# Optimization experiments

Measured on AMD Instinct MI355X. Metric: run time of the kernel, lower is better.

Reference implementation:

```python
import jax, jax.numpy as jnp
import numpy as np

N, E, C_IN, C_OUT, G = 100000, 1250000, 64, 64, 64
H = 2 * C_OUT  # hidden width of conv1 output


def _lin(k, out_d, in_d, scale=0.05):
    kw, kb = jax.random.split(k)
    return (jax.random.normal(kw, (out_d, in_d), jnp.float32) * scale,
            jax.random.normal(kb, (out_d,), jnp.float32) * scale)


def setup_inputs() -> dict:
    key = jax.random.key(0)
    ks = jax.random.split(key, 12)
    x = jax.random.normal(ks[0], (N, C_IN), jnp.float32)
    edge_index = jax.random.randint(ks[1], (2, E), 0, N, jnp.int64)
    batch = jnp.sort(jax.random.randint(ks[2], (N,), 0, G, jnp.int64))
    # GraphConv layer 1: lin_rel (with bias) on aggregated msgs, lin_root (no bias) on x
    w1_rel, b1_rel = _lin(ks[3], H, C_IN)
    w1_root = jax.random.normal(ks[4], (H, C_IN), jnp.float32) * 0.05
    # GraphConv layer 2
    w2_rel, b2_rel = _lin(ks[5], C_OUT, H)
    w2_root = jax.random.normal(ks[6], (C_OUT, H), jnp.float32) * 0.05
    # encoder_S: out_channels -> 8 -> 4 -> 1
    es_w1, es_b1 = _lin(ks[7], 8, C_OUT)
    es_w2, es_b2 = _lin(ks[8], 4, 8)
    es_w3, es_b3 = _lin(ks[9], 1, 4)
    # decoder: 1 -> 4 -> 8 -> out_channels (input dim fixed from buggy 2 to 1)
    d_w1, d_b1 = _lin(ks[10], 4, 1)
    d_w2, d_b2 = _lin(ks[11], 8, 4)
    d_w3, d_b3 = _lin(jax.random.fold_in(key, 99), C_OUT, 8)
    return dict(x=x, edge_index=edge_index, batch=batch,
                w1_rel=w1_rel, b1_rel=b1_rel, w1_root=w1_root,
                w2_rel=w2_rel, b2_rel=b2_rel, w2_root=w2_root,
                es_w1=es_w1, es_b1=es_b1, es_w2=es_w2, es_b2=es_b2,
                es_w3=es_w3, es_b3=es_b3,
                d_w1=d_w1, d_b1=d_b1, d_w2=d_w2, d_b2=d_b2,
                d_w3=d_w3, d_b3=d_b3)


def reference(x, edge_index, batch,
              w1_rel, b1_rel, w1_root,
              w2_rel, b2_rel, w2_root,
              es_w1, es_b1, es_w2, es_b2, es_w3, es_b3,
              d_w1, d_b1, d_w2, d_b2, d_w3, d_b3):
    src, dst = edge_index[0], edge_index[1]
    # GraphConv 1: sum-aggregate source feats into targets, then rel+root linears
    agg1 = jax.ops.segment_sum(x[src], dst, num_segments=N)  # [N, C_IN]
    h1 = jax.nn.relu(agg1 @ w1_rel.T + b1_rel + x @ w1_root.T)  # [N, H]
    # GraphConv 2
    agg2 = jax.ops.segment_sum(h1[src], dst, num_segments=N)
    h2 = jax.nn.relu(agg2 @ w2_rel.T + b2_rel + h1 @ w2_root.T)  # [N, C_OUT]
    # global mean pool over graphs
    counts = jax.ops.segment_sum(jnp.ones((N,), h2.dtype), batch, num_segments=G)
    h3 = jax.ops.segment_sum(h2, batch, num_segments=G) / jnp.maximum(counts, 1.0)[:, None]  # [G, C_OUT]
    # encoder_S MLP -> z
    z = jax.nn.relu(h3 @ es_w1.T + es_b1)
    z = jax.nn.relu(z @ es_w2.T + es_b2)
    z = z @ es_w3.T + es_b3  # [G, 1]
    # decoder MLP -> x_
    x_ = jax.nn.relu(z @ d_w1.T + d_b1)
    x_ = jax.nn.relu(x_ @ d_w2.T + d_b2)
    x_ = x_ @ d_w3.T + d_b3  # [G, C_OUT]
    return h3, x_
```

## Files before the change

kernel.cpp:

```cpp
#include <hip/hip_runtime.h>
#include <stdint.h>

#define NN 100000
#define EE 1250000
#define NBUCK 196
#define CHUNK 4096
#define NCHUNK ((EE + CHUNK - 1) / CHUNK)
#define PSLICE 24

typedef __attribute__((ext_vector_type(8))) short short8;
typedef __attribute__((ext_vector_type(4))) float f32x4;

__device__ inline ushort f2bf(float f) {
  union { float f; uint32_t u; } v; v.f = f;
  uint32_t r = v.u + 0x7FFF + ((v.u >> 16) & 1);
  return (ushort)(r >> 16);
}
__device__ inline float bf2f(ushort h) {
  union { uint32_t u; float f; } v; v.u = ((uint32_t)h) << 16;
  return v.f;
}

__global__ __launch_bounds__(256) void kprepfrag(const float* __restrict__ w1_rel,
                                                 const float* __restrict__ w1_root,
                                                 const float* __restrict__ w2_rel,
                                                 const float* __restrict__ w2_root,
                                                 ushort* __restrict__ WF) {
  int idx = blockIdx.x * 256 + threadIdx.x;
  if (idx >= 8192) return;
  int j = idx & 7, l = (idx >> 3) & 63, ts = idx >> 9;
  {
    int s = ts & 1, t = ts >> 1;
    int o = t * 16 + (l & 15), k = s * 32 + (l >> 4) * 8 + j;
    WF[idx] = f2bf(w1_rel[o * 64 + k]);
    WF[8192 + idx] = f2bf(w1_root[o * 64 + k]);
  }
  {
    int s = ts & 3, t = ts >> 2;
    int o = t * 16 + (l & 15), k = s * 32 + (l >> 4) * 8 + j;
    WF[16384 + idx] = f2bf(w2_rel[o * 128 + k]);
    WF[24576 + idx] = f2bf(w2_root[o * 128 + k]);
  }
}

__global__ __launch_bounds__(256) void kxcvt(const float* __restrict__ x,
                                             ushort* __restrict__ xb) {
  int i = (blockIdx.x * 256 + threadIdx.x) * 4;
  if (i >= NN * 64) return;
  float4 v = *reinterpret_cast<const float4*>(x + i);
  ushort o[4] = {f2bf(v.x), f2bf(v.y), f2bf(v.z), f2bf(v.w)};
  *reinterpret_cast<uint2*>(xb + i) = *reinterpret_cast<uint2*>(o);
}

__global__ __launch_bounds__(256) void kbinA1(const int* __restrict__ dstI,
                                              int* __restrict__ histG) {
  __shared__ int h[NBUCK];
  int t = threadIdx.x;
  if (t < NBUCK) h[t] = 0;
  __syncthreads();
  int cb = blockIdx.x * CHUNK;
  int cc = EE - cb; if (cc > CHUNK) cc = CHUNK;
  for (int i = t; i < cc; i += 256) atomicAdd(&h[dstI[cb + i] >> 9], 1);
  __syncthreads();
  if (t < NBUCK) histG[blockIdx.x * NBUCK + t] = h[t];
}

__global__ __launch_bounds__(512) void kscan2d(const int* __restrict__ histG,
                                               int* __restrict__ relG,
                                               int* __restrict__ bucketTotal) {
  __shared__ int sm[512];
  int b = blockIdx.x;
  int t = threadIdx.x;
  int v = (t < NCHUNK) ? histG[t * NBUCK + b] : 0;
  sm[t] = v;
  __syncthreads();
  for (int d = 1; d < 512; d <<= 1) {
    int u = (t >= d) ? sm[t - d] : 0;
    __syncthreads();
    sm[t] += u;
    __syncthreads();
  }
  if (t < NCHUNK) relG[t * NBUCK + b] = sm[t] - v;
  if (t == 511) bucketTotal[b] = sm[511];
}

__global__ __launch_bounds__(256) void kscan196(const int* __restrict__ bucketTotal,
                                                int* __restrict__ bucketStart) {
  __shared__ int ss[256];
  int t = threadIdx.x;
  int v = (t < NBUCK) ? bucketTotal[t] : 0;
  ss[t] = v;
  __syncthreads();
  for (int d = 1; d < 256; d <<= 1) {
    int u = (t >= d) ? ss[t - d] : 0;
    __syncthreads();
    ss[t] += u;
    __syncthreads();
  }
  if (t < NBUCK) bucketStart[t] = ss[t] - v;
  if (t == NBUCK - 1) bucketStart[NBUCK] = ss[t];
}

__global__ __launch_bounds__(256) void kbinA2(const int* __restrict__ srcI,
                                              const int* __restrict__ dstI,
                                              const int* __restrict__ histG,
                                              const int* __restrict__ relG,
                                              const int* __restrict__ bucketStart,
                                              uint32_t* __restrict__ pairsG) {
  __shared__ uint32_t pko[CHUNK];
  __shared__ int ss[256];
  __shared__ int ex[NBUCK + 1];
  __shared__ int cur[NBUCK];
  __shared__ int gb[NBUCK];
  int t = threadIdx.x;
  int cb = blockIdx.x * CHUNK;
  int cc = EE - cb; if (cc > CHUNK) cc = CHUNK;

  int v = (t < NBUCK) ? histG[blockIdx.x * NBUCK + t] : 0;
  ss[t] = v;
  __syncthreads();
  for (int d = 1; d < 256; d <<= 1) {
    int u = (t >= d) ? ss[t - d] : 0;
    __syncthreads();
    ss[t] += u;
    __syncthreads();
  }
  if (t < NBUCK) {
    ex[t] = ss[t] - v;
    cur[t] = ss[t] - v;
    gb[t] = bucketStart[t] + relG[blockIdx.x * NBUCK + t];
  }
  if (t == NBUCK - 1) ex[NBUCK] = ss[t];
  __syncthreads();
  for (int i = t; i < cc; i += 256) {
    int d = dstI[cb + i];
    int s = srcI[cb + i];
    int b = d >> 9;
    int p = atomicAdd(&cur[b], 1);
    pko[p] = (uint32_t)s | ((uint32_t)(d & 511) << 17);
  }
  __syncthreads();
  if (t < NBUCK) {
    int base = ex[t], cnt = ex[t + 1] - base, g0 = gb[t];
    for (int j = 0; j < cnt; ++j) pairsG[g0 + j] = pko[base + j];
  }
}

__global__ __launch_bounds__(256) void kbinB(const uint32_t* __restrict__ pairsG,
                                             const int* __restrict__ bucketStart,
                                             int* __restrict__ starts,
                                             int* __restrict__ esrc) {
  __shared__ int hist[512];
  __shared__ int ex2[512];
  __shared__ int part[256];
  int t = threadIdx.x;
  int b = blockIdx.x;
  int nbase = b << 9;
  int base = bucketStart[b];
  int ecnt = bucketStart[b + 1] - base;

  hist[t] = 0; hist[t + 256] = 0;
  __syncthreads();
  for (int i = t; i < ecnt; i += 256) atomicAdd(&hist[pairsG[base + i] >> 17], 1);
  __syncthreads();
  int a = hist[2 * t], c = hist[2 * t + 1];
  part[t] = a + c;
  __syncthreads();
  for (int d = 1; d < 256; d <<= 1) {
    int u = (t >= d) ? part[t - d] : 0;
    __syncthreads();
    part[t] += u;
    __syncthreads();
  }
  int pex = part[t] - (a + c);
  ex2[2 * t] = pex;
  ex2[2 * t + 1] = pex + a;
  __syncthreads();
  for (int n = t; n < 512; n += 256) {
    int node = nbase + n;
    if (node < NN) starts[node] = base + ex2[n];
  }
  if (b == NBUCK - 1 && t == 0) starts[NN] = EE;
  for (int n = t; n < 512; n += 256) hist[n] = ex2[n];
  __syncthreads();
  for (int i = t; i < ecnt; i += 256) {
    uint32_t p = pairsG[base + i];
    int dl = p >> 17;
    int s = p & 0x1FFFF;
    int lp = atomicAdd(&hist[dl], 1);
    esrc[base + lp] = s;
  }
}

__global__ __launch_bounds__(256) void kgatherQ(const ushort* __restrict__ featb,
                                                const int* __restrict__ starts,
                                                const int* __restrict__ esrc,
                                                ushort* __restrict__ outb) {
  int w = (blockIdx.x * 256 + threadIdx.x) >> 4;
  if (w >= NN) return;
  int lq = threadIdx.x & 15;
  int b = starts[w], e = starts[w + 1];
  float a0 = 0.f, a1 = 0.f, a2 = 0.f, a3 = 0.f;
  int i = b;
  int s0 = 0, s1 = 0, s2 = 0, s3 = 0;
  bool have = (i + 4 <= e);
  if (have) { s0 = esrc[i]; s1 = esrc[i + 1]; s2 = esrc[i + 2]; s3 = esrc[i + 3]; }
  while (have) {
    uint2 u0 = *(const uint2*)(featb + (size_t)s0 * 64 + 4 * lq);
    uint2 u1 = *(const uint2*)(featb + (size_t)s1 * 64 + 4 * lq);
    uint2 u2 = *(const uint2*)(featb + (size_t)s2 * 64 + 4 * lq);
    uint2 u3 = *(const uint2*)(featb + (size_t)s3 * 64 + 4 * lq);
    i += 4;
    have = (i + 4 <= e);
    if (have) { s0 = esrc[i]; s1 = esrc[i + 1]; s2 = esrc[i + 2]; s3 = esrc[i + 3]; }
    a0 += bf2f((ushort)u0.x) + bf2f((ushort)u1.x) + bf2f((ushort)u2.x) + bf2f((ushort)u3.x);
    a1 += bf2f((ushort)(u0.x >> 16)) + bf2f((ushort)(u1.x >> 16)) +
          bf2f((ushort)(u2.x >> 16)) + bf2f((ushort)(u3.x >> 16));
    a2 += bf2f((ushort)u0.y) + bf2f((ushort)u1.y) + bf2f((ushort)u2.y) + bf2f((ushort)u3.y);
    a3 += bf2f((ushort)(u0.y >> 16)) + bf2f((ushort)(u1.y >> 16)) +
          bf2f((ushort)(u2.y >> 16)) + bf2f((ushort)(u3.y >> 16));
  }
  for (; i < e; ++i) {
    int s = esrc[i];
    uint2 u = *(const uint2*)(featb + (size_t)s * 64 + 4 * lq);
    a0 += bf2f((ushort)u.x); a1 += bf2f((ushort)(u.x >> 16));
    a2 += bf2f((ushort)u.y); a3 += bf2f((ushort)(u.y >> 16));
  }
  uint2 o;
  o.x = (uint32_t)f2bf(a0) | ((uint32_t)f2bf(a1) << 16);
  o.y = (uint32_t)f2bf(a2) | ((uint32_t)f2bf(a3) << 16);
  *(uint2*)(outb + (size_t)w * 64 + 4 * lq) = o;
}

__global__ __launch_bounds__(256) void kgh2Q(const ushort* __restrict__ featb,
                                             const int* __restrict__ starts,
                                             const int* __restrict__ esrc,
                                             const ushort* __restrict__ r2b,
                                             const float* __restrict__ b2v,
                                             ushort* __restrict__ h2b) {
  int w = (blockIdx.x * 256 + threadIdx.x) >> 4;
  if (w >= NN) return;
  int lq = threadIdx.x & 15;
  int b = starts[w], e = starts[w + 1];
  float a0 = 0.f, a1 = 0.f, a2 = 0.f, a3 = 0.f;
  int i = b;
  int s0 = 0, s1 = 0, s2 = 0, s3 = 0;
  bool have = (i + 4 <= e);
  if (have) { s0 = esrc[i]; s1 = esrc[i + 1]; s2 = esrc[i + 2]; s3 = esrc[i + 3]; }
  while (have) {
    uint2 u0 = *(const uint2*)(featb + (size_t)s0 * 64 + 4 * lq);
    uint2 u1 = *(const uint2*)(featb + (size_t)s1 * 64 + 4 * lq);
    uint2 u2 = *(const uint2*)(featb + (size_t)s2 * 64 + 4 * lq);
    uint2 u3 = *(const uint2*)(featb + (size_t)s3 * 64 + 4 * lq);
    i += 4;
    have = (i + 4 <= e);
    if (have) { s0 = esrc[i]; s1 = esrc[i + 1]; s2 = esrc[i + 2]; s3 = esrc[i + 3]; }
    a0 += bf2f((ushort)u0.x) + bf2f((ushort)u1.x) + bf2f((ushort)u2.x) + bf2f((ushort)u3.x);
    a1 += bf2f((ushort)(u0.x >> 16)) + bf2f((ushort)(u1.x >> 16)) +
          bf2f((ushort)(u2.x >> 16)) + bf2f((ushort)(u3.x >> 16));
    a2 += bf2f((ushort)u0.y) + bf2f((ushort)u1.y) + bf2f((ushort)u2.y) + bf2f((ushort)u3.y);
    a3 += bf2f((ushort)(u0.y >> 16)) + bf2f((ushort)(u1.y >> 16)) +
          bf2f((ushort)(u2.y >> 16)) + bf2f((ushort)(u3.y >> 16));
  }
  for (; i < e; ++i) {
    int s = esrc[i];
    uint2 u = *(const uint2*)(featb + (size_t)s * 64 + 4 * lq);
    a0 += bf2f((ushort)u.x); a1 += bf2f((ushort)(u.x >> 16));
    a2 += bf2f((ushort)u.y); a3 += bf2f((ushort)(u.y >> 16));
  }
  uint2 ru = *(const uint2*)(r2b + (size_t)w * 64 + 4 * lq);
  float4 bias = *(const float4*)(b2v + 4 * lq);
  float v0 = fmaxf(a0 + bf2f((ushort)ru.x) + bias.x, 0.f);
  float v1 = fmaxf(a1 + bf2f((ushort)(ru.x >> 16)) + bias.y, 0.f);
  float v2 = fmaxf(a2 + bf2f((ushort)ru.y) + bias.z, 0.f);
  float v3 = fmaxf(a3 + bf2f((ushort)(ru.y >> 16)) + bias.w, 0.f);
  uint2 o;
  o.x = (uint32_t)f2bf(v0) | ((uint32_t)f2bf(v1) << 16);
  o.y = (uint32_t)f2bf(v2) | ((uint32_t)f2bf(v3) << 16);
  *(uint2*)(h2b + (size_t)w * 64 + 4 * lq) = o;
}

__global__ __launch_bounds__(256) void kfused(const ushort* __restrict__ xb,
                                              const ushort* __restrict__ aggb,
                                              const ushort* __restrict__ WF,
                                              const float* __restrict__ b1,
                                              ushort* __restrict__ y,
                                              ushort* __restrict__ r2b) {
  __shared__ __align__(16) char hT[16384];
  int t = threadIdx.x, l = t & 63, wv = t >> 6;
  int n0 = blockIdx.x * 64 + wv * 16;
  int row = l & 15;
  int kg = l >> 4;
  int nr = n0 + row; if (nr > NN - 1) nr = NN - 1;

  short8 aA[2], aX[2];
  {
    const ushort* ap = aggb + (size_t)nr * 64 + kg * 8;
    aA[0] = *(const short8*)(ap);
    aA[1] = *(const short8*)(ap + 32);
    const ushort* xp = xb + (size_t)nr * 64 + kg * 8;
    aX[0] = *(const short8*)(xp);
    aX[1] = *(const short8*)(xp + 32);
  }

  const ushort* wf1rel = WF;
  const ushort* wf1root = WF + 8192;
  char* basep = hT + wv * 4096;

#pragma unroll
  for (int tt = 0; tt < 8; ++tt) {
    f32x4 acc = {0.f, 0.f, 0.f, 0.f};
#pragma unroll
    for (int s = 0; s < 2; ++s) {
      short8 br = *(const short8*)(wf1rel + ((size_t)(tt * 2 + s) * 64 + l) * 8);
      acc = __builtin_amdgcn_mfma_f32_16x16x32_bf16(aA[s], br, acc, 0, 0, 0);
      short8 bo = *(const short8*)(wf1root + ((size_t)(tt * 2 + s) * 64 + l) * 8);
      acc = __builtin_amdgcn_mfma_f32_16x16x32_bf16(aX[s], bo, acc, 0, 0, 0);
    }
    float bias = b1[tt * 16 + row];
#pragma unroll
    for (int r = 0; r < 4; ++r) {
      float hv = fmaxf(acc[r] + bias, 0.f);
      int nl = kg * 4 + r;
      int off = nl * 256 + (tt * 16 + row) * 2;
      off ^= (nl & 7) << 4;
      *(ushort*)(basep + off) = f2bf(hv);
    }
  }
  __syncthreads();

  short8 aH[4];
#pragma unroll
  for (int s = 0; s < 4; ++s) {
    int off = row * 256 + s * 64 + kg * 16;
    off ^= (row & 7) << 4;
    aH[s] = *(const short8*)(basep + off);
  }

  const ushort* wf2rel = WF + 16384;
  const ushort* wf2root = WF + 24576;
#pragma unroll
  for (int tt = 0; tt < 4; ++tt) {
    f32x4 accY = {0.f, 0.f, 0.f, 0.f};
    f32x4 accR = {0.f, 0.f, 0.f, 0.f};
#pragma unroll
    for (int s = 0; s < 4; ++s) {
      short8 br = *(const short8*)(wf2rel + ((size_t)(tt * 4 + s) * 64 + l) * 8);
      accY = __builtin_amdgcn_mfma_f32_16x16x32_bf16(aH[s], br, accY, 0, 0, 0);
      short8 bo = *(const short8*)(wf2root + ((size_t)(tt * 4 + s) * 64 + l) * 8);
      accR = __builtin_amdgcn_mfma_f32_16x16x32_bf16(aH[s], bo, accR, 0, 0, 0);
    }
#pragma unroll
    for (int r = 0; r < 4; ++r) {
      int nd = n0 + kg * 4 + r;
      if (nd < NN) {
        y[(size_t)nd * 64 + tt * 16 + row] = f2bf(accY[r]);
        r2b[(size_t)nd * 64 + tt * 16 + row] = f2bf(accR[r]);
      }
    }
  }
}

__global__ __launch_bounds__(256) void kpoolpart(const ushort* __restrict__ h2b,
                                                 const int* __restrict__ batch,
                                                 float* __restrict__ poolP) {
  __shared__ int gbs[2];
  __shared__ float part[4][64];
  int g = blockIdx.x / PSLICE, sl = blockIdx.x % PSLICE;
  int t = threadIdx.x;
  if (t < 2) {
    int target = g + t;
    int lo = 0, hi = NN;
    while (lo < hi) { int m = (lo + hi) >> 1; if (batch[m] < target) lo = m + 1; else hi = m; }
    gbs[t] = lo;
  }
  __syncthreads();
  int n0 = gbs[0], len = gbs[1] - n0;
  int lo = n0 + (int)((long)len * sl / PSLICE);
  int hi = n0 + (int)((long)len * (sl + 1) / PSLICE);
  int ch = t & 63, sub = t >> 6;
  float acc = 0.f;
  int n = lo + sub;
  for (; n + 12 < hi; n += 16) {
    float v0 = bf2f(h2b[(size_t)n * 64 + ch]);
    float v1 = bf2f(h2b[(size_t)(n + 4) * 64 + ch]);
    float v2 = bf2f(h2b[(size_t)(n + 8) * 64 + ch]);
    float v3 = bf2f(h2b[(size_t)(n + 12) * 64 + ch]);
    acc += (v0 + v1) + (v2 + v3);
  }
  for (; n < hi; n += 4) acc += bf2f(h2b[(size_t)n * 64 + ch]);
  part[sub][ch] = acc;
  __syncthreads();
  if (t < 64)
    poolP[(size_t)blockIdx.x * 64 + t] = part[0][t] + part[1][t] + part[2][t] + part[3][t];
}

__global__ __launch_bounds__(64) void kfinal3(
    const float* __restrict__ poolP, const int* __restrict__ batch,
    const float* __restrict__ es_w1, const float* __restrict__ es_b1,
    const float* __restrict__ es_w2, const float* __restrict__ es_b2,
    const float* __restrict__ es_w3, const float* __restrict__ es_b3,
    const float* __restrict__ d_w1, const float* __restrict__ d_b1,
    const float* __restrict__ d_w2, const float* __restrict__ d_b2,
    const float* __restrict__ d_w3, const float* __restrict__ d_b3,
    float* __restrict__ out) {
  __shared__ float h3[64];
  __shared__ float z1s[8];
  __shared__ float t2s[8];
  __shared__ int gbs[2];
  int g = blockIdx.x;
  int l = threadIdx.x;
  if (l < 2) {
    int target = g + l;
    int lo = 0, hi = NN;
    while (lo < hi) { int m = (lo + hi) >> 1; if (batch[m] < target) lo = m + 1; else hi = m; }
    gbs[l] = lo;
  }
  float s = 0.f;
#pragma unroll
  for (int k = 0; k < PSLICE; ++k) s += poolP[(size_t)(g * PSLICE + k) * 64 + l];
  __syncthreads();
  float c = fmaxf((float)(gbs[1] - gbs[0]), 1.f);
  float h = s / c;
  h3[l] = h;
  out[g * 64 + l] = h;
  __syncthreads();
  if (l < 8) {
    float a = es_b1[l];
#pragma unroll
    for (int k = 0; k < 64; ++k) a += es_w1[l * 64 + k] * h3[k];
    z1s[l] = fmaxf(a, 0.f);
  }
  __syncthreads();
  if (l == 0) {
    float z2[4];
#pragma unroll
    for (int j = 0; j < 4; ++j) {
      float a = es_b2[j];
#pragma unroll
      for (int k = 0; k < 8; ++k) a += es_w2[j * 8 + k] * z1s[k];
      z2[j] = fmaxf(a, 0.f);
    }
    float z = es_b3[0];
#pragma unroll
    for (int k = 0; k < 4; ++k) z += es_w3[k] * z2[k];
    float t1[4];
#pragma unroll
    for (int j = 0; j < 4; ++j) t1[j] = fmaxf(d_w1[j] * z + d_b1[j], 0.f);
#pragma unroll
    for (int j = 0; j < 8; ++j) {
      float a = d_b2[j];
#pragma unroll
      for (int k = 0; k < 4; ++k) a += d_w2[j * 4 + k] * t1[k];
      t2s[j] = fmaxf(a, 0.f);
    }
  }
  __syncthreads();
  float a = d_b3[l];
#pragma unroll
  for (int k = 0; k < 8; ++k) a += d_w3[l * 8 + k] * t2s[k];
  out[4096 + g * 64 + l] = a;
}

extern "C" void kernel_launch(void* const* d_in, const int* in_sizes, int n_in,
                              void* d_out, int out_size, void* d_ws, size_t ws_size,
                              hipStream_t stream) {
  const float* x = (const float*)d_in[0];
  const int* ei = (const int*)d_in[1];
  const int* srcI = ei;
  const int* dstI = ei + EE;
  const int* batch = (const int*)d_in[2];
  const float* w1_rel = (const float*)d_in[3];
  const float* b1_rel = (const float*)d_in[4];
  const float* w1_root = (const float*)d_in[5];
  const float* w2_rel = (const float*)d_in[6];
  const float* b2_rel = (const float*)d_in[7];
  const float* w2_root = (const float*)d_in[8];
  const float* es_w1 = (const float*)d_in[9];
  const float* es_b1 = (const float*)d_in[10];
  const float* es_w2 = (const float*)d_in[11];
  const float* es_b2 = (const float*)d_in[12];
  const float* es_w3 = (const float*)d_in[13];
  const float* es_b3 = (const float*)d_in[14];
  const float* d_w1 = (const float*)d_in[15];
  const float* d_b1 = (const float*)d_in[16];
  const float* d_w2 = (const float*)d_in[17];
  const float* d_b2 = (const float*)d_in[18];
  const float* d_w3 = (const float*)d_in[19];
  const float* d_b3 = (const float*)d_in[20];

  ushort* xb = (ushort*)d_ws;
  ushort* aggb = xb + (size_t)NN * 64;
  ushort* yb = aggb + (size_t)NN * 64;
  ushort* r2b = yb + (size_t)NN * 64;
  ushort* h2b = r2b + (size_t)NN * 64;
  ushort* WF = h2b + (size_t)NN * 64;
  float* poolP = (float*)(WF + 32768);
  int* starts = (int*)(poolP + 64 * PSLICE * 64);
  int* histG = starts + NN + 1;
  int* relG = histG + NCHUNK * NBUCK;
  int* bucketTotal = relG + NCHUNK * NBUCK;
  int* bucketStart = bucketTotal + NBUCK;
  uint32_t* pairsG = (uint32_t*)(bucketStart + NBUCK + 1);
  int* esrc = (int*)(pairsG + EE);
  float* out = (float*)d_out;

  kprepfrag<<<32, 256, 0, stream>>>(w1_rel, w1_root, w2_rel, w2_root, WF);
  kxcvt<<<(NN * 64 / 4 + 255) / 256, 256, 0, stream>>>(x, xb);
  kbinA1<<<NCHUNK, 256, 0, stream>>>(dstI, histG);
  kscan2d<<<NBUCK, 512, 0, stream>>>(histG, relG, bucketTotal);
  kscan196<<<1, 256, 0, stream>>>(bucketTotal, bucketStart);
  kbinA2<<<NCHUNK, 256, 0, stream>>>(srcI, dstI, histG, relG, bucketStart, pairsG);
  kbinB<<<NBUCK, 256, 0, stream>>>(pairsG, bucketStart, starts, esrc);
  kgatherQ<<<(NN * 16 + 255) / 256, 256, 0, stream>>>(xb, starts, esrc, aggb);
  kfused<<<(NN + 63) / 64, 256, 0, stream>>>(xb, aggb, WF, b1_rel, yb, r2b);
  kgh2Q<<<(NN * 16 + 255) / 256, 256, 0, stream>>>(yb, starts, esrc, r2b, b2_rel, h2b);
  kpoolpart<<<64 * PSLICE, 256, 0, stream>>>(h2b, batch, poolP);
  kfinal3<<<64, 64, 0, stream>>>(poolP, batch, es_w1, es_b1, es_w2, es_b2, es_w3, es_b3,
                                 d_w1, d_b1, d_w2, d_b2, d_w3, d_b3, out);
}
```

Baseline: 148.9 us.

## Merge front-end prep kernels, deepen gather unroll, double rows per wave in kfused

Folds the weight-fragment prep, x-to-bf16 conversion and destination histogram kernels into one launch that dispatches on block index, removing two kernel launches and their gaps. The two gather kernels share a macro that prefetches eight edge indices per iteration and handles the tail in 4/2/1 steps, raising memory-level parallelism per lane. The fused MLP kernel now processes 32 rows per wave with a 32KB LDS buffer, reusing each loaded weight fragment twice at the cost of more registers and LDS, which may reduce occupancy.

```diff
diff --git a/kernel.cpp b/kernel.cpp
--- a/kernel.cpp
+++ b/kernel.cpp
@@ -7,6 +7,7 @@
 #define CHUNK 4096
 #define NCHUNK ((EE + CHUNK - 1) / CHUNK)
 #define PSLICE 24
+#define XB_NB ((NN * 64 / 4 + 255) / 256)
 
 typedef __attribute__((ext_vector_type(8))) short short8;
 typedef __attribute__((ext_vector_type(4))) float f32x4;
@@ -21,48 +22,52 @@
   return v.f;
 }
 
-__global__ __launch_bounds__(256) void kprepfrag(const float* __restrict__ w1_rel,
-                                                 const float* __restrict__ w1_root,
-                                                 const float* __restrict__ w2_rel,
-                                                 const float* __restrict__ w2_root,
-                                                 ushort* __restrict__ WF) {
-  int idx = blockIdx.x * 256 + threadIdx.x;
-  if (idx >= 8192) return;
-  int j = idx & 7, l = (idx >> 3) & 63, ts = idx >> 9;
-  {
-    int s = ts & 1, t = ts >> 1;
-    int o = t * 16 + (l & 15), k = s * 32 + (l >> 4) * 8 + j;
-    WF[idx] = f2bf(w1_rel[o * 64 + k]);
-    WF[8192 + idx] = f2bf(w1_root[o * 64 + k]);
-  }
-  {
-    int s = ts & 3, t = ts >> 2;
-    int o = t * 16 + (l & 15), k = s * 32 + (l >> 4) * 8 + j;
-    WF[16384 + idx] = f2bf(w2_rel[o * 128 + k]);
-    WF[24576 + idx] = f2bf(w2_root[o * 128 + k]);
-  }
-}
-
-__global__ __launch_bounds__(256) void kxcvt(const float* __restrict__ x,
-                                             ushort* __restrict__ xb) {
-  int i = (blockIdx.x * 256 + threadIdx.x) * 4;
-  if (i >= NN * 64) return;
-  float4 v = *reinterpret_cast<const float4*>(x + i);
-  ushort o[4] = {f2bf(v.x), f2bf(v.y), f2bf(v.z), f2bf(v.w)};
-  *reinterpret_cast<uint2*>(xb + i) = *reinterpret_cast<uint2*>(o);
-}
-
-__global__ __launch_bounds__(256) void kbinA1(const int* __restrict__ dstI,
+__global__ __launch_bounds__(256) void kfront(const float* __restrict__ w1_rel,
+                                              const float* __restrict__ w1_root,
+                                              const float* __restrict__ w2_rel,
+                                              const float* __restrict__ w2_root,
+                                              const float* __restrict__ x,
+                                              const int* __restrict__ dstI,
+                                              ushort* __restrict__ WF,
+                                              ushort* __restrict__ xb,
                                               int* __restrict__ histG) {
   __shared__ int h[NBUCK];
   int t = threadIdx.x;
-  if (t < NBUCK) h[t] = 0;
-  __syncthreads();
-  int cb = blockIdx.x * CHUNK;
-  int cc = EE - cb; if (cc > CHUNK) cc = CHUNK;
-  for (int i = t; i < cc; i += 256) atomicAdd(&h[dstI[cb + i] >> 9], 1);
-  __syncthreads();
-  if (t < NBUCK) histG[blockIdx.x * NBUCK + t] = h[t];
+  int blk = blockIdx.x;
+  if (blk < 32) {
+    int idx = blk * 256 + t;
+    if (idx < 8192) {
+      int j = idx & 7, l = (idx >> 3) & 63, ts = idx >> 9;
+      {
+        int s = ts & 1, tt = ts >> 1;
+        int o = tt * 16 + (l & 15), k = s * 32 + (l >> 4) * 8 + j;
+        WF[idx] = f2bf(w1_rel[o * 64 + k]);
+        WF[8192 + idx] = f2bf(w1_root[o * 64 + k]);
+      }
+      {
+        int s = ts & 3, tt = ts >> 2;
+        int o = tt * 16 + (l & 15), k = s * 32 + (l >> 4) * 8 + j;
+        WF[16384 + idx] = f2bf(w2_rel[o * 128 + k]);
+        WF[24576 + idx] = f2bf(w2_root[o * 128 + k]);
+      }
+    }
+  } else if (blk < 32 + XB_NB) {
+    int i = ((blk - 32) * 256 + t) * 4;
+    if (i < NN * 64) {
+      float4 v = *reinterpret_cast<const float4*>(x + i);
+      ushort o[4] = {f2bf(v.x), f2bf(v.y), f2bf(v.z), f2bf(v.w)};
+      *reinterpret_cast<uint2*>(xb + i) = *reinterpret_cast<uint2*>(o);
+    }
+  } else {
+    int c = blk - 32 - XB_NB;
+    if (t < NBUCK) h[t] = 0;
+    __syncthreads();
+    int cb = c * CHUNK;
+    int cc = EE - cb; if (cc > CHUNK) cc = CHUNK;
+    for (int i = t; i < cc; i += 256) atomicAdd(&h[dstI[cb + i] >> 9], 1);
+    __syncthreads();
+    if (t < NBUCK) histG[c * NBUCK + t] = h[t];
+  }
 }
 
 __global__ __launch_bounds__(512) void kscan2d(const int* __restrict__ histG,
@@ -192,6 +197,79 @@
   }
 }
 
+#define GATHER_CORE(featb)                                                         \
+  float a0 = 0.f, a1 = 0.f, a2 = 0.f, a3 = 0.f;                                    \
+  const ushort* fb = (featb) + 4 * lq;                                             \
+  int i = b;                                                                       \
+  {                                                                                \
+    int s0 = 0, s1 = 0, s2 = 0, s3 = 0, s4 = 0, s5 = 0, s6 = 0, s7 = 0;            \
+    bool have = (i + 8 <= e);                                                      \
+    if (have) {                                                                    \
+      s0 = esrc[i];     s1 = esrc[i + 1]; s2 = esrc[i + 2]; s3 = esrc[i + 3];      \
+      s4 = esrc[i + 4]; s5 = esrc[i + 5]; s6 = esrc[i + 6]; s7 = esrc[i + 7];      \
+    }                                                                              \
+    while (have) {                                                                 \
+      uint2 u0 = *(const uint2*)(fb + (size_t)s0 * 64);                            \
+      uint2 u1 = *(const uint2*)(fb + (size_t)s1 * 64);                            \
+      uint2 u2 = *(const uint2*)(fb + (size_t)s2 * 64);                            \
+      uint2 u3 = *(const uint2*)(fb + (size_t)s3 * 64);                            \
+      uint2 u4 = *(const uint2*)(fb + (size_t)s4 * 64);                            \
+      uint2 u5 = *(const uint2*)(fb + (size_t)s5 * 64);                            \
+      uint2 u6 = *(const uint2*)(fb + (size_t)s6 * 64);                            \
+      uint2 u7 = *(const uint2*)(fb + (size_t)s7 * 64);                            \
+      i += 8;                                                                      \
+      have = (i + 8 <= e);                                                         \
+      if (have) {                                                                  \
+        s0 = esrc[i];     s1 = esrc[i + 1]; s2 = esrc[i + 2]; s3 = esrc[i + 3];    \
+        s4 = esrc[i + 4]; s5 = esrc[i + 5]; s6 = esrc[i + 6]; s7 = esrc[i + 7];    \
+      }                                                                            \
+      a0 += bf2f((ushort)u0.x) + bf2f((ushort)u1.x) + bf2f((ushort)u2.x) +         \
+            bf2f((ushort)u3.x) + bf2f((ushort)u4.x) + bf2f((ushort)u5.x) +         \
+            bf2f((ushort)u6.x) + bf2f((ushort)u7.x);                               \
+      a1 += bf2f((ushort)(u0.x >> 16)) + bf2f((ushort)(u1.x >> 16)) +              \
+            bf2f((ushort)(u2.x >> 16)) + bf2f((ushort)(u3.x >> 16)) +              \
+            bf2f((ushort)(u4.x >> 16)) + bf2f((ushort)(u5.x >> 16)) +              \
+            bf2f((ushort)(u6.x >> 16)) + bf2f((ushort)(u7.x >> 16));               \
+      a2 += bf2f((ushort)u0.y) + bf2f((ushort)u1.y) + bf2f((ushort)u2.y) +         \
+            bf2f((ushort)u3.y) + bf2f((ushort)u4.y) + bf2f((ushort)u5.y) +         \
+            bf2f((ushort)u6.y) + bf2f((ushort)u7.y);                               \
+      a3 += bf2f((ushort)(u0.y >> 16)) + bf2f((ushort)(u1.y >> 16)) +              \
+            bf2f((ushort)(u2.y >> 16)) + bf2f((ushort)(u3.y >> 16)) +              \
+            bf2f((ushort)(u4.y >> 16)) + bf2f((ushort)(u5.y >> 16)) +              \
+            bf2f((ushort)(u6.y >> 16)) + bf2f((ushort)(u7.y >> 16));               \
+    }                                                                              \
+  }                                                                                \
+  if (i + 4 <= e) {                                                                \
+    int s0 = esrc[i], s1 = esrc[i + 1], s2 = esrc[i + 2], s3 = esrc[i + 3];        \
+    uint2 u0 = *(const uint2*)(fb + (size_t)s0 * 64);                              \
+    uint2 u1 = *(const uint2*)(fb + (size_t)s1 * 64);                              \
+    uint2 u2 = *(const uint2*)(fb + (size_t)s2 * 64);                              \
+    uint2 u3 = *(const uint2*)(fb + (size_t)s3 * 64);                              \
+    a0 += bf2f((ushort)u0.x) + bf2f((ushort)u1.x) + bf2f((ushort)u2.x) + bf2f((ushort)u3.x); \
+    a1 += bf2f((ushort)(u0.x >> 16)) + bf2f((ushort)(u1.x >> 16)) +                \
+          bf2f((ushort)(u2.x >> 16)) + bf2f((ushort)(u3.x >> 16));                 \
+    a2 += bf2f((ushort)u0.y) + bf2f((ushort)u1.y) + bf2f((ushort)u2.y) + bf2f((ushort)u3.y); \
+    a3 += bf2f((ushort)(u0.y >> 16)) + bf2f((ushort)(u1.y >> 16)) +                \
+          bf2f((ushort)(u2.y >> 16)) + bf2f((ushort)(u3.y >> 16));                 \
+    i += 4;                                                                        \
+  }                                                                                \
+  if (i + 2 <= e) {                                                                \
+    int s0 = esrc[i], s1 = esrc[i + 1];                                            \
+    uint2 u0 = *(const uint2*)(fb + (size_t)s0 * 64);                              \
+    uint2 u1 = *(const uint2*)(fb + (size_t)s1 * 64);                              \
+    a0 += bf2f((ushort)u0.x) + bf2f((ushort)u1.x);                                 \
+    a1 += bf2f((ushort)(u0.x >> 16)) + bf2f((ushort)(u1.x >> 16));                 \
+    a2 += bf2f((ushort)u0.y) + bf2f((ushort)u1.y);                                 \
+    a3 += bf2f((ushort)(u0.y >> 16)) + bf2f((ushort)(u1.y >> 16));                 \
+    i += 2;                                                                        \
+  }                                                                                \
+  if (i < e) {                                                                     \
+    int s0 = esrc[i];                                                              \
+    uint2 u0 = *(const uint2*)(fb + (size_t)s0 * 64);                              \
+    a0 += bf2f((ushort)u0.x); a1 += bf2f((ushort)(u0.x >> 16));                    \
+    a2 += bf2f((ushort)u0.y); a3 += bf2f((ushort)(u0.y >> 16));                    \
+  }
+
 __global__ __launch_bounds__(256) void kgatherQ(const ushort* __restrict__ featb,
                                                 const int* __restrict__ starts,
                                                 const int* __restrict__ esrc,
@@ -200,32 +278,7 @@
   if (w >= NN) return;
   int lq = threadIdx.x & 15;
   int b = starts[w], e = starts[w + 1];
-  float a0 = 0.f, a1 = 0.f, a2 = 0.f, a3 = 0.f;
-  int i = b;
-  int s0 = 0, s1 = 0, s2 = 0, s3 = 0;
-  bool have = (i + 4 <= e);
-  if (have) { s0 = esrc[i]; s1 = esrc[i + 1]; s2 = esrc[i + 2]; s3 = esrc[i + 3]; }
-  while (have) {
-    uint2 u0 = *(const uint2*)(featb + (size_t)s0 * 64 + 4 * lq);
-    uint2 u1 = *(const uint2*)(featb + (size_t)s1 * 64 + 4 * lq);
-    uint2 u2 = *(const uint2*)(featb + (size_t)s2 * 64 + 4 * lq);
-    uint2 u3 = *(const uint2*)(featb + (size_t)s3 * 64 + 4 * lq);
-    i += 4;
-    have = (i + 4 <= e);
-    if (have) { s0 = esrc[i]; s1 = esrc[i + 1]; s2 = esrc[i + 2]; s3 = esrc[i + 3]; }
-    a0 += bf2f((ushort)u0.x) + bf2f((ushort)u1.x) + bf2f((ushort)u2.x) + bf2f((ushort)u3.x);
-    a1 += bf2f((ushort)(u0.x >> 16)) + bf2f((ushort)(u1.x >> 16)) +
-          bf2f((ushort)(u2.x >> 16)) + bf2f((ushort)(u3.x >> 16));
-    a2 += bf2f((ushort)u0.y) + bf2f((ushort)u1.y) + bf2f((ushort)u2.y) + bf2f((ushort)u3.y);
-    a3 += bf2f((ushort)(u0.y >> 16)) + bf2f((ushort)(u1.y >> 16)) +
-          bf2f((ushort)(u2.y >> 16)) + bf2f((ushort)(u3.y >> 16));
-  }
-  for (; i < e; ++i) {
-    int s = esrc[i];
-    uint2 u = *(const uint2*)(featb + (size_t)s * 64 + 4 * lq);
-    a0 += bf2f((ushort)u.x); a1 += bf2f((ushort)(u.x >> 16));
-    a2 += bf2f((ushort)u.y); a3 += bf2f((ushort)(u.y >> 16));
-  }
+  GATHER_CORE(featb)
   uint2 o;
   o.x = (uint32_t)f2bf(a0) | ((uint32_t)f2bf(a1) << 16);
   o.y = (uint32_t)f2bf(a2) | ((uint32_t)f2bf(a3) << 16);
@@ -242,32 +295,7 @@
   if (w >= NN) return;
   int lq = threadIdx.x & 15;
   int b = starts[w], e = starts[w + 1];
-  float a0 = 0.f, a1 = 0.f, a2 = 0.f, a3 = 0.f;
-  int i = b;
-  int s0 = 0, s1 = 0, s2 = 0, s3 = 0;
-  bool have = (i + 4 <= e);
-  if (have) { s0 = esrc[i]; s1 = esrc[i + 1]; s2 = esrc[i + 2]; s3 = esrc[i + 3]; }
-  while (have) {
-    uint2 u0 = *(const uint2*)(featb + (size_t)s0 * 64 + 4 * lq);
-    uint2 u1 = *(const uint2*)(featb + (size_t)s1 * 64 + 4 * lq);
-    uint2 u2 = *(const uint2*)(featb + (size_t)s2 * 64 + 4 * lq);
-    uint2 u3 = *(const uint2*)(featb + (size_t)s3 * 64 + 4 * lq);
-    i += 4;
-    have = (i + 4 <= e);
-    if (have) { s0 = esrc[i]; s1 = esrc[i + 1]; s2 = esrc[i + 2]; s3 = esrc[i + 3]; }
-    a0 += bf2f((ushort)u0.x) + bf2f((ushort)u1.x) + bf2f((ushort)u2.x) + bf2f((ushort)u3.x);
-    a1 += bf2f((ushort)(u0.x >> 16)) + bf2f((ushort)(u1.x >> 16)) +
-          bf2f((ushort)(u2.x >> 16)) + bf2f((ushort)(u3.x >> 16));
-    a2 += bf2f((ushort)u0.y) + bf2f((ushort)u1.y) + bf2f((ushort)u2.y) + bf2f((ushort)u3.y);
-    a3 += bf2f((ushort)(u0.y >> 16)) + bf2f((ushort)(u1.y >> 16)) +
-          bf2f((ushort)(u2.y >> 16)) + bf2f((ushort)(u3.y >> 16));
-  }
-  for (; i < e; ++i) {
-    int s = esrc[i];
-    uint2 u = *(const uint2*)(featb + (size_t)s * 64 + 4 * lq);
-    a0 += bf2f((ushort)u.x); a1 += bf2f((ushort)(u.x >> 16));
-    a2 += bf2f((ushort)u.y); a3 += bf2f((ushort)(u.y >> 16));
-  }
+  GATHER_CORE(featb)
   uint2 ru = *(const uint2*)(r2b + (size_t)w * 64 + 4 * lq);
   float4 bias = *(const float4*)(b2v + 4 * lq);
   float v0 = fmaxf(a0 + bf2f((ushort)ru.x) + bias.x, 0.f);
@@ -286,76 +314,97 @@
                                               const float* __restrict__ b1,
                                               ushort* __restrict__ y,
                                               ushort* __restrict__ r2b) {
-  __shared__ __align__(16) char hT[16384];
+  __shared__ __align__(16) char hT[32768];
   int t = threadIdx.x, l = t & 63, wv = t >> 6;
-  int n0 = blockIdx.x * 64 + wv * 16;
+  int n0 = blockIdx.x * 128 + wv * 32;
   int row = l & 15;
   int kg = l >> 4;
-  int nr = n0 + row; if (nr > NN - 1) nr = NN - 1;
-
-  short8 aA[2], aX[2];
+  int nr0 = n0 + row;      if (nr0 > NN - 1) nr0 = NN - 1;
+  int nr1 = n0 + 16 + row; if (nr1 > NN - 1) nr1 = NN - 1;
+
+  short8 aA0[2], aX0[2], aA1[2], aX1[2];
   {
-    const ushort* ap = aggb + (size_t)nr * 64 + kg * 8;
-    aA[0] = *(const short8*)(ap);
-    aA[1] = *(const short8*)(ap + 32);
-    const ushort* xp = xb + (size_t)nr * 64 + kg * 8;
-    aX[0] = *(const short8*)(xp);
-    aX[1] = *(const short8*)(xp + 32);
+    const ushort* ap0 = aggb + (size_t)nr0 * 64 + kg * 8;
+    aA0[0] = *(const short8*)(ap0);
+    aA0[1] = *(const short8*)(ap0 + 32);
+    const ushort* xp0 = xb + (size_t)nr0 * 64 + kg * 8;
+    aX0[0] = *(const short8*)(xp0);
+    aX0[1] = *(const short8*)(xp0 + 32);
+    const ushort* ap1 = aggb + (size_t)nr1 * 64 + kg * 8;
+    aA1[0] = *(const short8*)(ap1);
+    aA1[1] = *(const short8*)(ap1 + 32);
+    const ushort* xp1 = xb + (size_t)nr1 * 64 + kg * 8;
+    aX1[0] = *(const short8*)(xp1);
+    aX1[1] = *(const short8*)(xp1 + 32);
   }
 
   const ushort* wf1rel = WF;
   const ushort* wf1root = WF + 8192;
-  char* basep = hT + wv * 4096;
+  char* base0 = hT + wv * 8192;
+  char* base1 = base0 + 4096;
 
 #pragma unroll
   for (int tt = 0; tt < 8; ++tt) {
-    f32x4 acc = {0.f, 0.f, 0.f, 0.f};
+    f32x4 acc0 = {0.f, 0.f, 0.f, 0.f};
+    f32x4 acc1 = {0.f, 0.f, 0.f, 0.f};
 #pragma unroll
     for (int s = 0; s < 2; ++s) {
       short8 br = *(const short8*)(wf1rel + ((size_t)(tt * 2 + s) * 64 + l) * 8);
-      acc = __builtin_amdgcn_mfma_f32_16x16x32_bf16(aA[s], br, acc, 0, 0, 0);
       short8 bo = *(const short8*)(wf1root + ((size_t)(tt * 2 + s) * 64 + l) * 8);
-      acc = __builtin_amdgcn_mfma_f32_16x16x32_bf16(aX[s], bo, acc, 0, 0, 0);
+      acc0 = __builtin_amdgcn_mfma_f32_16x16x32_bf16(aA0[s], br, acc0, 0, 0, 0);
+      acc0 = __builtin_amdgcn_mfma_f32_16x16x32_bf16(aX0[s], bo, acc0, 0, 0, 0);
+      acc1 = __builtin_amdgcn_mfma_f32_16x16x32_bf16(aA1[s], br, acc1, 0, 0, 0);
+      acc1 = __builtin_amdgcn_mfma_f32_16x16x32_bf16(aX1[s], bo, acc1, 0, 0, 0);
     }
     float bias = b1[tt * 16 + row];
 #pragma unroll
     for (int r = 0; r < 4; ++r) {
-      float hv = fmaxf(acc[r] + bias, 0.f);
       int nl = kg * 4 + r;
       int off = nl * 256 + (tt * 16 + row) * 2;
       off ^= (nl & 7) << 4;
-      *(ushort*)(basep + off) = f2bf(hv);
-    }
-  }
-  __syncthreads();
-
-  short8 aH[4];
+      *(ushort*)(base0 + off) = f2bf(fmaxf(acc0[r] + bias, 0.f));
+      *(ushort*)(base1 + off) = f2bf(fmaxf(acc1[r] + bias, 0.f));
+    }
+  }
+  __syncthreads();
+
+  short8 aH0[4], aH1[4];
 #pragma unroll
   for (int s = 0; s < 4; ++s) {
     int off = row * 256 + s * 64 + kg * 16;
     off ^= (row & 7) << 4;
-    aH[s] = *(const short8*)(basep + off);
+    aH0[s] = *(const short8*)(base0 + off);
+    aH1[s] = *(const short8*)(base1 + off);
   }
 
   const ushort* wf2rel = WF + 16384;
   const ushort* wf2root = WF + 24576;
 #pragma unroll
   for (int tt = 0; tt < 4; ++tt) {
-    f32x4 accY = {0.f, 0.f, 0.f, 0.f};
-    f32x4 accR = {0.f, 0.f, 0.f, 0.f};
+    f32x4 accY0 = {0.f, 0.f, 0.f, 0.f};
+    f32x4 accR0 = {0.f, 0.f, 0.f, 0.f};
+    f32x4 accY1 = {0.f, 0.f, 0.f, 0.f};
+    f32x4 accR1 = {0.f, 0.f, 0.f, 0.f};
 #pragma unroll
     for (int s = 0; s < 4; ++s) {
       short8 br = *(const short8*)(wf2rel + ((size_t)(tt * 4 + s) * 64 + l) * 8);
-      accY = __builtin_amdgcn_mfma_f32_16x16x32_bf16(aH[s], br, accY, 0, 0, 0);
       short8 bo = *(const short8*)(wf2root + ((size_t)(tt * 4 + s) * 64 + l) * 8);
-      accR = __builtin_amdgcn_mfma_f32_16x16x32_bf16(aH[s], bo, accR, 0, 0, 0);
+      accY0 = __builtin_amdgcn_mfma_f32_16x16x32_bf16(aH0[s], br, accY0, 0, 0, 0);
+      accR0 = __builtin_amdgcn_mfma_f32_16x16x32_bf16(aH0[s], bo, accR0, 0, 0, 0);
+      accY1 = __builtin_amdgcn_mfma_f32_16x16x32_bf16(aH1[s], br, accY1, 0, 0, 0);
+      accR1 = __builtin_amdgcn_mfma_f32_16x16x32_bf16(aH1[s], bo, accR1, 0, 0, 0);
     }
 #pragma unroll
     for (int r = 0; r < 4; ++r) {
-      int nd = n0 + kg * 4 + r;
-      if (nd < NN) {
-        y[(size_t)nd * 64 + tt * 16 + row] = f2bf(accY[r]);
-        r2b[(size_t)nd * 64 + tt * 16 + row] = f2bf(accR[r]);
+      int nd0 = n0 + kg * 4 + r;
+      int nd1 = nd0 + 16;
+      if (nd0 < NN) {
+        y[(size_t)nd0 * 64 + tt * 16 + row] = f2bf(accY0[r]);
+        r2b[(size_t)nd0 * 64 + tt * 16 + row] = f2bf(accR0[r]);
+      }
+      if (nd1 < NN) {
+        y[(size_t)nd1 * 64 + tt * 16 + row] = f2bf(accY1[r]);
+        r2b[(size_t)nd1 * 64 + tt * 16 + row] = f2bf(accR1[r]);
       }
     }
   }
@@ -505,15 +554,14 @@
   int* esrc = (int*)(pairsG + EE);
   float* out = (float*)d_out;
 
-  kprepfrag<<<32, 256, 0, stream>>>(w1_rel, w1_root, w2_rel, w2_root, WF);
-  kxcvt<<<(NN * 64 / 4 + 255) / 256, 256, 0, stream>>>(x, xb);
-  kbinA1<<<NCHUNK, 256, 0, stream>>>(dstI, histG);
+  kfront<<<32 + XB_NB + NCHUNK, 256, 0, stream>>>(w1_rel, w1_root, w2_rel, w2_root,
+                                                  x, dstI, WF, xb, histG);
   kscan2d<<<NBUCK, 512, 0, stream>>>(histG, relG, bucketTotal);
   kscan196<<<1, 256, 0, stream>>>(bucketTotal, bucketStart);
   kbinA2<<<NCHUNK, 256, 0, stream>>>(srcI, dstI, histG, relG, bucketStart, pairsG);
   kbinB<<<NBUCK, 256, 0, stream>>>(pairsG, bucketStart, starts, esrc);
   kgatherQ<<<(NN * 16 + 255) / 256, 256, 0, stream>>>(xb, starts, esrc, aggb);
-  kfused<<<(NN + 63) / 64, 256, 0, stream>>>(xb, aggb, WF, b1_rel, yb, r2b);
+  kfused<<<(NN + 127) / 128, 256, 0, stream>>>(xb, aggb, WF, b1_rel, yb, r2b);
   kgh2Q<<<(NN * 16 + 255) / 256, 256, 0, stream>>>(yb, starts, esrc, r2b, b2_rel, h2b);
   kpoolpart<<<64 * PSLICE, 256, 0, stream>>>(h2b, batch, poolP);
   kfinal3<<<64, 64, 0, stream>>>(poolP, batch, es_w1, es_b1, es_w2, es_b2, es_w3, es_b3,
```

After: 139.6 us. 6.3% less time.
